# Performance work log

Hardware: AMD Instinct MI355X
Metric: run time of the kernel (lower is better)

## Reference

```python
import jax, jax.numpy as jnp
import numpy as np

N = 50000      # total nodes
E = 800000     # edges (before self loops)
B = 512        # graphs in batch
NODE_F = 9
GLOB_F = 4
IN_F = 13
H = 4          # heads
C = 16         # per-head channels (64 // 4)
HID = 64
NEG_SLOPE = 0.2


def setup_inputs() -> dict:
    key = jax.random.key(0)
    ks = jax.random.split(key, 32)
    inp = {}
    inp["node_feats"] = jax.random.normal(ks[0], (N, NODE_F), jnp.float32)
    inp["x_global_features"] = jax.random.normal(ks[1], (B, GLOB_F), jnp.float32)
    inp["edge_index"] = jax.random.randint(ks[2], (2, E), 0, N, jnp.int32)
    inp["batch_idx"] = jnp.sort(jax.random.randint(ks[3], (N,), 0, B, jnp.int32))
    dims = [IN_F, HID, HID]
    k = 4
    for l in range(3):
        s = 1.0 / np.sqrt(dims[l])
        inp[f"W{l}"] = jax.random.normal(ks[k], (dims[l], H * C), jnp.float32) * s; k += 1
        inp[f"att_src{l}"] = jax.random.normal(ks[k], (H, C), jnp.float32) * 0.1; k += 1
        inp[f"att_dst{l}"] = jax.random.normal(ks[k], (H, C), jnp.float32) * 0.1; k += 1
        inp[f"b{l}"] = jnp.zeros((H * C,), jnp.float32)
    mlp_dims = [(64, 64), (64, 64), (64, 64), (64, 1)]
    for i, (a, o) in enumerate(mlp_dims):
        inp[f"mlp_W{i}"] = jax.random.normal(ks[k], (a, o), jnp.float32) * (1.0 / np.sqrt(a)); k += 1
        inp[f"mlp_b{i}"] = jnp.zeros((o,), jnp.float32)
    return inp


def _gat_conv(x, src, dst, W, a_src, a_dst, bias, n):
    # h: [n, H, C]
    h = (x @ W).reshape(n, H, C)
    alpha_src = jnp.sum(h * a_src, axis=-1)   # [n, H]
    alpha_dst = jnp.sum(h * a_dst, axis=-1)   # [n, H]
    e = alpha_src[src] + alpha_dst[dst]       # [E', H]
    e = jax.nn.leaky_relu(e, NEG_SLOPE)
    # softmax over incoming edges per destination node (self loops guarantee >=1 edge)
    m = jax.ops.segment_max(e, dst, num_segments=n)
    e = jnp.exp(e - m[dst])
    s = jax.ops.segment_sum(e, dst, num_segments=n)
    alpha = e / s[dst]                        # [E', H]
    out = jax.ops.segment_sum(h[src] * alpha[:, :, None], dst, num_segments=n)
    return out.reshape(n, H * C) + bias


def _forward(node_feats, x_global_features,
             W0, att_src0, att_dst0, b0,
             W1, att_src1, att_dst1, b1,
             W2, att_src2, att_dst2, b2,
             mlp_W0, mlp_b0, mlp_W1, mlp_b1, mlp_W2, mlp_b2, mlp_W3, mlp_b3,
             edge_index, batch_idx):
    n = node_feats.shape[0]
    # concat per-graph global features onto each node
    x = jnp.concatenate([node_feats, x_global_features[batch_idx]], axis=1)  # [N, 13]
    loops = jnp.arange(n, dtype=edge_index.dtype)
    src = jnp.concatenate([edge_index[0], loops])
    dst = jnp.concatenate([edge_index[1], loops])
    x = jax.nn.relu(_gat_conv(x, src, dst, W0, att_src0, att_dst0, b0, n))
    x = jax.nn.relu(_gat_conv(x, src, dst, W1, att_src1, att_dst1, b1, n))
    x = _gat_conv(x, src, dst, W2, att_src2, att_dst2, b2, n)  # no act on last layer
    # scatter_mean over graphs
    sums = jax.ops.segment_sum(x, batch_idx, num_segments=B)
    cnt = jax.ops.segment_sum(jnp.ones((n,), x.dtype), batch_idx, num_segments=B)
    pooled = sums / jnp.clip(cnt, 1.0)[:, None]               # [B, 64]
    h = jax.nn.relu(pooled @ mlp_W0 + mlp_b0)
    h = jax.nn.relu(h @ mlp_W1 + mlp_b1)
    h = jax.nn.relu(h @ mlp_W2 + mlp_b2)
    out = h @ mlp_W3 + mlp_b3                                  # [B, 1]
    return out.reshape(-1)                                     # flatten -> [B]


def reference(node_feats, x_global_features,
              W0, att_src0, att_dst0, b0,
              W1, att_src1, att_dst1, b1,
              W2, att_src2, att_dst2, b2,
              mlp_W0, mlp_b0, mlp_W1, mlp_b1, mlp_W2, mlp_b2, mlp_W3, mlp_b3,
              edge_index, batch_idx):
    return _forward(node_feats, x_global_features,
                    W0, att_src0, att_dst0, b0,
                    W1, att_src1, att_dst1, b1,
                    W2, att_src2, att_dst2, b2,
                    mlp_W0, mlp_b0, mlp_W1, mlp_b1, mlp_W2, mlp_b2, mlp_W3, mlp_b3,
                    edge_index, batch_idx)
```

## Files before the change

kernel.cpp:

```cpp
#include <hip/hip_runtime.h>
#include <hip/hip_fp16.h>

#define GAT_H 4
#define GAT_HC 64
#define NEG_SLOPE 0.2f
#define DB 128
#define NBMAX 512
#define CHUNK 4096
#define EPT 16

__device__ __forceinline__ float lrelu(float x) { return x >= 0.f ? x : NEG_SLOPE * x; }

template <int K, bool CONCAT>
__global__ __launch_bounds__(256) void gemm_attn(
    const float* __restrict__ x, const float* __restrict__ nf,
    const float* __restrict__ gf, const int* __restrict__ batch,
    const float* __restrict__ W,
    const float* __restrict__ att_s, const float* __restrict__ att_d,
    __half* __restrict__ h, float* __restrict__ asrc, float* __restrict__ adst,
    int N, int nwaves)
{
    int lane = threadIdx.x & 63;
    int wid = blockIdx.x * 4 + __builtin_amdgcn_readfirstlane(threadIdx.x >> 6);

    float w[K];
    #pragma unroll
    for (int k = 0; k < K; ++k) w[k] = W[k * 64 + lane];
    float as_c = att_s[lane];
    float ad_c = att_d[lane];

    for (int row = wid; row < N; row += nwaves) {
        float acc = 0.f;
        if (CONCAT) {
            #pragma unroll
            for (int k = 0; k < 9; ++k) acc = fmaf(nf[row * 9 + k], w[k], acc);
            int b = batch[row];
            #pragma unroll
            for (int k = 0; k < 4; ++k) acc = fmaf(gf[b * 4 + k], w[9 + k], acc);
        } else {
            #pragma unroll
            for (int k = 0; k < K; ++k) acc = fmaf(x[(size_t)row * K + k], w[k], acc);
        }
        h[(unsigned)row * 64u + (unsigned)lane] = __float2half(acc);
        float vs = acc * as_c;
        float vd = acc * ad_c;
        #pragma unroll
        for (int off = 8; off; off >>= 1) { vs += __shfl_xor(vs, off); vd += __shfl_xor(vd, off); }
        if ((lane & 15) == 0) {
            asrc[row * GAT_H + (lane >> 4)] = vs;
            adst[row * GAT_H + (lane >> 4)] = vd;
        }
    }
}


__global__ __launch_bounds__(256) void zero_small(unsigned* __restrict__ bin_cnt,
                                                  unsigned* __restrict__ bin_fill)
{
    int t = threadIdx.x;
    bin_cnt[t] = 0; bin_cnt[t + 256] = 0;
    bin_fill[t] = 0; bin_fill[t + 256] = 0;
}

__global__ __launch_bounds__(256) void hist_bins(const int* __restrict__ dst,
                                                 unsigned* __restrict__ bin_cnt, int E)
{
    __shared__ unsigned lh[NBMAX];
    int t = threadIdx.x;
    lh[t] = 0; lh[t + 256] = 0;
    __syncthreads();
    for (int e = blockIdx.x * 256 + t; e < E; e += gridDim.x * 256)
        atomicAdd(&lh[((unsigned)dst[e]) >> 7], 1u);
    __syncthreads();
    unsigned v = lh[t];       if (v) atomicAdd(&bin_cnt[t], v);
    v = lh[t + 256];          if (v) atomicAdd(&bin_cnt[t + 256], v);
}

__global__ __launch_bounds__(256) void scan_bins(const unsigned* __restrict__ bin_cnt,
                                                 unsigned* __restrict__ bin_base,
                                                 int* __restrict__ indptr,
                                                 int nb, int N, int E)
{
    __shared__ unsigned buf[NBMAX];
    int t = threadIdx.x;
    buf[t] = (t < nb) ? bin_cnt[t] : 0u;
    buf[t + 256] = (t + 256 < nb) ? bin_cnt[t + 256] : 0u;
    __syncthreads();
    for (int off = 1; off < NBMAX; off <<= 1) {
        unsigned a = 0, b = 0;
        if (t >= off) a = buf[t - off];
        b = buf[t + 256 - off];
        __syncthreads();
        buf[t] += a; buf[t + 256] += b;
        __syncthreads();
    }
    if (t == 0) { bin_base[0] = 0; indptr[N] = E; }
    if (t < nb) bin_base[t + 1] = buf[t];
    if (t + 256 < nb) bin_base[t + 257] = buf[t + 256];
}

__global__ __launch_bounds__(256) void bin_scatter(const int* __restrict__ src,
                                                   const int* __restrict__ dst,
                                                   const unsigned* __restrict__ bin_base,
                                                   unsigned* __restrict__ bin_fill,
                                                   unsigned* __restrict__ binned, int E)
{
    __shared__ unsigned lh[NBMAX];
    __shared__ int goff[NBMAX];
    __shared__ unsigned sorted[CHUNK];
    int t = threadIdx.x;
    lh[t] = 0; lh[t + 256] = 0;
    __syncthreads();
    int e0 = blockIdx.x * CHUNK;

    unsigned pk[EPT]; int bn[EPT]; unsigned rk[EPT];
    #pragma unroll
    for (int i = 0; i < EPT; ++i) {
        int e = e0 + i * 256 + t;
        bn[i] = -1;
        if (e < E) {
            unsigned d = (unsigned)dst[e];
            pk[i] = (d << 16) | (unsigned)src[e];
            bn[i] = (int)(d >> 7);
            rk[i] = atomicAdd(&lh[bn[i]], 1u);
        }
    }
    __syncthreads();
    unsigned c0 = lh[t], c1 = lh[t + 256];
    for (int off = 1; off < NBMAX; off <<= 1) {
        unsigned a = 0, b = 0;
        if (t >= off) a = lh[t - off];
        b = lh[t + 256 - off];
        __syncthreads();
        lh[t] += a; lh[t + 256] += b;
        __syncthreads();
    }
    unsigned x0 = lh[t] - c0, x1 = lh[t + 256] - c1;
    if (c0) { unsigned g = atomicAdd(&bin_fill[t], c0);
              goff[t] = (int)(bin_base[t] + g) - (int)x0; }
    if (c1) { unsigned g = atomicAdd(&bin_fill[t + 256], c1);
              goff[t + 256] = (int)(bin_base[t + 256] + g) - (int)x1; }
    lh[t] = x0; lh[t + 256] = x1;
    __syncthreads();
    #pragma unroll
    for (int i = 0; i < EPT; ++i)
        if (bn[i] >= 0) sorted[lh[bn[i]] + rk[i]] = pk[i];
    __syncthreads();
    int T = min(CHUNK, E - e0);
    for (int j = t; j < T; j += 256) {
        unsigned p = sorted[j];
        binned[goff[p >> 23] + j] = p;
    }
}

__global__ __launch_bounds__(256) void bin_finalize(const unsigned* __restrict__ binned,
                                                    const unsigned* __restrict__ bin_base,
                                                    int* __restrict__ csr_src,
                                                    int* __restrict__ indptr, int N)
{
    __shared__ unsigned lh[DB];
    __shared__ unsigned fill[DB];
    int t = threadIdx.x, b = blockIdx.x;
    unsigned base = bin_base[b];
    unsigned cnt = bin_base[b + 1] - base;
    if (t < DB) lh[t] = 0;
    __syncthreads();
    for (unsigned i = t; i < cnt; i += 256)
        atomicAdd(&lh[(binned[base + i] >> 16) & (DB - 1)], 1u);
    __syncthreads();
    unsigned c0 = (t < DB) ? lh[t] : 0;
    for (int off = 1; off < DB; off <<= 1) {
        unsigned a = 0;
        if (t >= off && t < DB) a = lh[t - off];
        __syncthreads();
        if (t < DB) lh[t] += a;
        __syncthreads();
    }
    if (t < DB) {
        unsigned excl = lh[t] - c0;
        int d = b * DB + t;
        if (d < N) indptr[d] = (int)(base + excl);
        fill[t] = excl;
    }
    __syncthreads();
    for (unsigned i = t; i < cnt; i += 256) {
        unsigned p = binned[base + i];
        unsigned pos = atomicAdd(&fill[(p >> 16) & (DB - 1)], 1u);
        csr_src[base + pos] = (int)(p & 0xFFFFu);
    }
}

template <bool RELU>
__global__ __launch_bounds__(256) void aggregate(
    const __half* __restrict__ h, const float* __restrict__ asrc,
    const float* __restrict__ adst, const int* __restrict__ indptr,
    const int* __restrict__ csr_src, const float* __restrict__ bias,
    float* __restrict__ xout, int N, int nwaves)
{
    int lane = threadIdx.x & 63;
    int wid = blockIdx.x * 4 + __builtin_amdgcn_readfirstlane(threadIdx.x >> 6);
    unsigned h16 = (unsigned)(lane >> 4);
    float bias_c = bias[lane];

    for (int node = wid; node < N; node += nwaves) {
        int beg = __builtin_amdgcn_readfirstlane(indptr[node]);
        int end = __builtin_amdgcn_readfirstlane(indptr[node + 1]);
        unsigned un = (unsigned)node;

        float adst_n = adst[un * 4u + h16];
        float p0 = __expf(lrelu(asrc[un * 4u + h16] + adst_n));
        float sacc = p0;
        float acc = __half2float(h[un * 64u + (unsigned)lane]) * p0;

        int e = beg;
        for (; e + 16 <= end; e += 16) {
            int s[16]; float a[16], hv[16];
            #pragma unroll
            for (int i = 0; i < 16; ++i) s[i] = csr_src[e + i];
            #pragma unroll
            for (int i = 0; i < 16; ++i) a[i] = asrc[(unsigned)s[i] * 4u + h16];
            #pragma unroll
            for (int i = 0; i < 16; ++i)
                hv[i] = __half2float(h[(unsigned)s[i] * 64u + (unsigned)lane]);
            #pragma unroll
            for (int i = 0; i < 16; ++i) {
                float p = __expf(lrelu(a[i] + adst_n));
                sacc += p;
                acc = fmaf(hv[i], p, acc);
            }
        }
        for (; e + 8 <= end; e += 8) {
            int s[8]; float a[8], hv[8];
            #pragma unroll
            for (int i = 0; i < 8; ++i) s[i] = csr_src[e + i];
            #pragma unroll
            for (int i = 0; i < 8; ++i) a[i] = asrc[(unsigned)s[i] * 4u + h16];
            #pragma unroll
            for (int i = 0; i < 8; ++i)
                hv[i] = __half2float(h[(unsigned)s[i] * 64u + (unsigned)lane]);
            #pragma unroll
            for (int i = 0; i < 8; ++i) {
                float p = __expf(lrelu(a[i] + adst_n));
                sacc += p;
                acc = fmaf(hv[i], p, acc);
            }
        }
        for (; e + 2 <= end; e += 2) {
            int s0 = csr_src[e], s1 = csr_src[e + 1];
            float a0 = asrc[(unsigned)s0 * 4u + h16];
            float a1 = asrc[(unsigned)s1 * 4u + h16];
            float h0 = __half2float(h[(unsigned)s0 * 64u + (unsigned)lane]);
            float h1 = __half2float(h[(unsigned)s1 * 64u + (unsigned)lane]);
            float pa = __expf(lrelu(a0 + adst_n));
            float pb = __expf(lrelu(a1 + adst_n));
            sacc += pa + pb;
            acc = fmaf(h0, pa, acc);
            acc = fmaf(h1, pb, acc);
        }
        if (e < end) {
            int s = csr_src[e];
            float p = __expf(lrelu(asrc[(unsigned)s * 4u + h16] + adst_n));
            sacc += p;
            acc = fmaf(__half2float(h[(unsigned)s * 64u + (unsigned)lane]), p, acc);
        }

        float o = acc / sacc + bias_c;
        if (RELU) o = fmaxf(o, 0.f);
        xout[un * 64u + (unsigned)lane] = o;
    }
}

__global__ void pool_mlp(const float* __restrict__ x, const int* __restrict__ batch, int N,
                         const float* __restrict__ W0, const float* __restrict__ b0,
                         const float* __restrict__ W1, const float* __restrict__ b1,
                         const float* __restrict__ W2, const float* __restrict__ b2,
                         const float* __restrict__ W3, const float* __restrict__ b3,
                         float* __restrict__ out)
{
    __shared__ int bounds[2];
    __shared__ float red[4][64];
    __shared__ float hb[64];
    int b = blockIdx.x, t = threadIdx.x;

    if (t < 2) {
        int target = b + t;
        int lo = 0, hi = N;
        while (lo < hi) {
            int mid = (lo + hi) >> 1;
            if (batch[mid] < target) lo = mid + 1; else hi = mid;
        }
        bounds[t] = lo;
    }
    __syncthreads();
    int beg = bounds[0], end = bounds[1];

    int c = t & 63, w = t >> 6;
    float sum = 0.f;
    for (int n = beg + w; n < end; n += 4) sum += x[(size_t)n * 64 + c];
    red[w][c] = sum;
    __syncthreads();
    if (t < 64) {
        float v = red[0][t] + red[1][t] + red[2][t] + red[3][t];
        float cb = fmaxf((float)(end - beg), 1.0f);
        hb[t] = v / cb;
    }
    __syncthreads();

    float v0 = 0.f;
    if (t < 64) {
        v0 = b0[t];
        for (int k = 0; k < 64; ++k) v0 = fmaf(hb[k], W0[k * 64 + t], v0);
        v0 = fmaxf(v0, 0.f);
    }
    __syncthreads(); if (t < 64) hb[t] = v0; __syncthreads();
    if (t < 64) {
        v0 = b1[t];
        for (int k = 0; k < 64; ++k) v0 = fmaf(hb[k], W1[k * 64 + t], v0);
        v0 = fmaxf(v0, 0.f);
    }
    __syncthreads(); if (t < 64) hb[t] = v0; __syncthreads();
    if (t < 64) {
        v0 = b2[t];
        for (int k = 0; k < 64; ++k) v0 = fmaf(hb[k], W2[k * 64 + t], v0);
        v0 = fmaxf(v0, 0.f);
    }
    __syncthreads(); if (t < 64) hb[t] = v0; __syncthreads();
    if (t < 64) {
        float r = hb[t] * W3[t];
        #pragma unroll
        for (int off = 32; off; off >>= 1) r += __shfl_xor(r, off);
        if (t == 0) out[b] = r + b3[0];
    }
}

extern "C" void kernel_launch(void* const* d_in, const int* in_sizes, int n_in,
                              void* d_out, int out_size, void* d_ws, size_t ws_size,
                              hipStream_t stream)
{
    const float* node_feats = (const float*)d_in[0];
    const float* glob       = (const float*)d_in[1];
    const int*   edge_index = (const int*)d_in[2];
    const int*   batch      = (const int*)d_in[3];
    const float* W[3]  = {(const float*)d_in[4],  (const float*)d_in[8],  (const float*)d_in[12]};
    const float* As[3] = {(const float*)d_in[5],  (const float*)d_in[9],  (const float*)d_in[13]};
    const float* Ad[3] = {(const float*)d_in[6],  (const float*)d_in[10], (const float*)d_in[14]};
    const float* Bi[3] = {(const float*)d_in[7],  (const float*)d_in[11], (const float*)d_in[15]};
    const float* mW0 = (const float*)d_in[16]; const float* mb0 = (const float*)d_in[17];
    const float* mW1 = (const float*)d_in[18]; const float* mb1 = (const float*)d_in[19];
    const float* mW2 = (const float*)d_in[20]; const float* mb2 = (const float*)d_in[21];
    const float* mW3 = (const float*)d_in[22]; const float* mb3 = (const float*)d_in[23];
    float* out = (float*)d_out;

    int N = in_sizes[0] / 9;
    int E = in_sizes[2] / 2;
    int B = in_sizes[1] / 4;
    const int* esrc = edge_index;
    const int* edst = edge_index + E;
    int nb = (N + DB - 1) / DB;

    char* ws = (char*)d_ws;
    size_t off = 0;
    auto alloc = [&](size_t bytes) -> void* {
        void* p = ws + off;
        off = (off + bytes + 255) & ~(size_t)255;
        return p;
    };
    __half*   hbuf     = (__half*)alloc((size_t)N * 64 * 2);
    float*    xbuf     = (float*)alloc((size_t)N * 64 * 4);
    float*    asrc     = (float*)alloc((size_t)N * GAT_H * 4);
    float*    adst     = (float*)alloc((size_t)N * GAT_H * 4);
    int*      indptr   = (int*)alloc((size_t)(N + 1) * 4);
    int*      csr_src  = (int*)alloc((size_t)E * 4);
    unsigned* binned   = (unsigned*)alloc((size_t)E * 4);
    unsigned* bin_cnt  = (unsigned*)alloc(NBMAX * 4);
    unsigned* bin_base = (unsigned*)alloc((NBMAX + 1) * 4);
    unsigned* bin_fill = (unsigned*)alloc(NBMAX * 4);
    (void)ws_size;

    zero_small<<<1, 256, 0, stream>>>(bin_cnt, bin_fill);
    hist_bins<<<400, 256, 0, stream>>>(edst, bin_cnt, E);
    scan_bins<<<1, 256, 0, stream>>>(bin_cnt, bin_base, indptr, nb, N, E);
    bin_scatter<<<(E + CHUNK - 1) / CHUNK, 256, 0, stream>>>(esrc, edst, bin_base, bin_fill,
                                                             binned, E);
    bin_finalize<<<nb, 256, 0, stream>>>(binned, bin_base, csr_src, indptr, N);

    const int gemmBlocks = 1024;
    const int aggBlocks = 12500;
    gemm_attn<13, true><<<gemmBlocks, 256, 0, stream>>>(nullptr, node_feats, glob, batch,
                                                        W[0], As[0], Ad[0], hbuf, asrc, adst,
                                                        N, gemmBlocks * 4);
    aggregate<true><<<aggBlocks, 256, 0, stream>>>(hbuf, asrc, adst, indptr, csr_src, Bi[0],
                                                   xbuf, N, aggBlocks * 4);
    gemm_attn<64, false><<<gemmBlocks, 256, 0, stream>>>(xbuf, nullptr, nullptr, nullptr,
                                                         W[1], As[1], Ad[1], hbuf, asrc, adst,
                                                         N, gemmBlocks * 4);
    aggregate<true><<<aggBlocks, 256, 0, stream>>>(hbuf, asrc, adst, indptr, csr_src, Bi[1],
                                                   xbuf, N, aggBlocks * 4);
    gemm_attn<64, false><<<gemmBlocks, 256, 0, stream>>>(xbuf, nullptr, nullptr, nullptr,
                                                         W[2], As[2], Ad[2], hbuf, asrc, adst,
                                                         N, gemmBlocks * 4);
    aggregate<false><<<aggBlocks, 256, 0, stream>>>(hbuf, asrc, adst, indptr, csr_src, Bi[2],
                                                    xbuf, N, aggBlocks * 4);

    pool_mlp<<<B, 256, 0, stream>>>(xbuf, batch, N,
                                    mW0, mb0, mW1, mb1, mW2, mb2, mW3, mb3, out);
}
```

Measured before the change: 184.6 us.

## Process eight edges per wave in aggregation and drop global atomics in histogram

```diff
diff --git a/kernel.cpp b/kernel.cpp
--- a/kernel.cpp
+++ b/kernel.cpp
@@ -8,6 +8,7 @@
 #define NBMAX 512
 #define CHUNK 4096
 #define EPT 16
+#define SLICES 128
 
 __device__ __forceinline__ float lrelu(float x) { return x >= 0.f ? x : NEG_SLOPE * x; }
 
@@ -54,16 +55,8 @@
 }
 
 
-__global__ __launch_bounds__(256) void zero_small(unsigned* __restrict__ bin_cnt,
-                                                  unsigned* __restrict__ bin_fill)
-{
-    int t = threadIdx.x;
-    bin_cnt[t] = 0; bin_cnt[t + 256] = 0;
-    bin_fill[t] = 0; bin_fill[t + 256] = 0;
-}
-
 __global__ __launch_bounds__(256) void hist_bins(const int* __restrict__ dst,
-                                                 unsigned* __restrict__ bin_cnt, int E)
+                                                 unsigned* __restrict__ slices, int E)
 {
     __shared__ unsigned lh[NBMAX];
     int t = threadIdx.x;
@@ -72,19 +65,26 @@
     for (int e = blockIdx.x * 256 + t; e < E; e += gridDim.x * 256)
         atomicAdd(&lh[((unsigned)dst[e]) >> 7], 1u);
     __syncthreads();
-    unsigned v = lh[t];       if (v) atomicAdd(&bin_cnt[t], v);
-    v = lh[t + 256];          if (v) atomicAdd(&bin_cnt[t + 256], v);
-}
-
-__global__ __launch_bounds__(256) void scan_bins(const unsigned* __restrict__ bin_cnt,
+    unsigned* slice = slices + (size_t)blockIdx.x * NBMAX;
+    slice[t] = lh[t];
+    slice[t + 256] = lh[t + 256];
+}
+
+__global__ __launch_bounds__(256) void scan_bins(const unsigned* __restrict__ slices,
                                                  unsigned* __restrict__ bin_base,
+                                                 unsigned* __restrict__ bin_fill,
                                                  int* __restrict__ indptr,
-                                                 int nb, int N, int E)
+                                                 int nslices, int N, int E)
 {
     __shared__ unsigned buf[NBMAX];
     int t = threadIdx.x;
-    buf[t] = (t < nb) ? bin_cnt[t] : 0u;
-    buf[t + 256] = (t + 256 < nb) ? bin_cnt[t + 256] : 0u;
+    unsigned s0 = 0, s1 = 0;
+    for (int s = 0; s < nslices; ++s) {
+        s0 += slices[(size_t)s * NBMAX + t];
+        s1 += slices[(size_t)s * NBMAX + t + 256];
+    }
+    buf[t] = s0; buf[t + 256] = s1;
+    bin_fill[t] = 0; bin_fill[t + 256] = 0;
     __syncthreads();
     for (int off = 1; off < NBMAX; off <<= 1) {
         unsigned a = 0, b = 0;
@@ -95,8 +95,8 @@
         __syncthreads();
     }
     if (t == 0) { bin_base[0] = 0; indptr[N] = E; }
-    if (t < nb) bin_base[t + 1] = buf[t];
-    if (t + 256 < nb) bin_base[t + 257] = buf[t + 256];
+    bin_base[t + 1] = buf[t];
+    bin_base[t + 257] = buf[t + 256];
 }
 
 __global__ __launch_bounds__(256) void bin_scatter(const int* __restrict__ src,
@@ -187,6 +187,107 @@
         unsigned p = binned[base + i];
         unsigned pos = atomicAdd(&fill[(p >> 16) & (DB - 1)], 1u);
         csr_src[base + pos] = (int)(p & 0xFFFFu);
+    }
+}
+
+template <bool RELU>
+__global__ __launch_bounds__(256) void aggregate8(
+    const __half* __restrict__ h, const float* __restrict__ asrc,
+    const float* __restrict__ adst, const int* __restrict__ indptr,
+    const int* __restrict__ csr_src, const float* __restrict__ bias,
+    float* __restrict__ xout, int N, int nwaves)
+{
+    int lane = threadIdx.x & 63;
+    int eslot = lane >> 3;
+    unsigned c8 = (unsigned)(lane & 7);
+    unsigned head = c8 >> 1;
+    int wid = blockIdx.x * 4 + __builtin_amdgcn_readfirstlane(threadIdx.x >> 6);
+
+    float4 bias0 = *reinterpret_cast<const float4*>(bias + c8 * 8u);
+    float4 bias1 = *reinterpret_cast<const float4*>(bias + c8 * 8u + 4u);
+
+    for (int node = wid; node < N; node += nwaves) {
+        int beg = __builtin_amdgcn_readfirstlane(indptr[node]);
+        int end = __builtin_amdgcn_readfirstlane(indptr[node + 1]);
+        int total = (end - beg) + 1;
+
+        float adst_n = adst[(unsigned)node * 4u + head];
+        float sacc = 0.f;
+        float acc[8];
+        #pragma unroll
+        for (int j = 0; j < 8; ++j) acc[j] = 0.f;
+
+        int g = 0;
+        for (; g + 16 <= total; g += 16) {
+            int i0 = g + eslot;
+            int i1 = g + 8 + eslot;
+            int s0 = (i0 == 0) ? node : csr_src[beg + i0 - 1];
+            int s1 = csr_src[beg + i1 - 1];
+            float a0 = asrc[(unsigned)s0 * 4u + head];
+            float a1 = asrc[(unsigned)s1 * 4u + head];
+            uint4 hv0 = *reinterpret_cast<const uint4*>(h + (unsigned)s0 * 64u + c8 * 8u);
+            uint4 hv1 = *reinterpret_cast<const uint4*>(h + (unsigned)s1 * 64u + c8 * 8u);
+            float p0 = __expf(lrelu(a0 + adst_n));
+            float p1 = __expf(lrelu(a1 + adst_n));
+            sacc += p0 + p1;
+            const __half2* q0 = reinterpret_cast<const __half2*>(&hv0);
+            const __half2* q1 = reinterpret_cast<const __half2*>(&hv1);
+            #pragma unroll
+            for (int j = 0; j < 4; ++j) {
+                float2 f0 = __half22float2(q0[j]);
+                float2 f1 = __half22float2(q1[j]);
+                acc[2 * j]     = fmaf(f0.x, p0, acc[2 * j]);
+                acc[2 * j + 1] = fmaf(f0.y, p0, acc[2 * j + 1]);
+                acc[2 * j]     = fmaf(f1.x, p1, acc[2 * j]);
+                acc[2 * j + 1] = fmaf(f1.y, p1, acc[2 * j + 1]);
+            }
+        }
+        for (; g < total; g += 8) {
+            int idx = g + eslot;
+            if (idx < total) {
+                int s = (idx == 0) ? node : csr_src[beg + idx - 1];
+                float a = asrc[(unsigned)s * 4u + head];
+                uint4 hv = *reinterpret_cast<const uint4*>(h + (unsigned)s * 64u + c8 * 8u);
+                float p = __expf(lrelu(a + adst_n));
+                sacc += p;
+                const __half2* q = reinterpret_cast<const __half2*>(&hv);
+                #pragma unroll
+                for (int j = 0; j < 4; ++j) {
+                    float2 f = __half22float2(q[j]);
+                    acc[2 * j]     = fmaf(f.x, p, acc[2 * j]);
+                    acc[2 * j + 1] = fmaf(f.y, p, acc[2 * j + 1]);
+                }
+            }
+        }
+
+        #pragma unroll
+        for (int off = 8; off <= 32; off <<= 1) {
+            sacc += __shfl_xor(sacc, off);
+            #pragma unroll
+            for (int j = 0; j < 8; ++j) acc[j] += __shfl_xor(acc[j], off);
+        }
+
+        if (eslot == 0) {
+            float inv = 1.0f / sacc;
+            float4 o0, o1;
+            o0.x = fmaf(acc[0], inv, bias0.x);
+            o0.y = fmaf(acc[1], inv, bias0.y);
+            o0.z = fmaf(acc[2], inv, bias0.z);
+            o0.w = fmaf(acc[3], inv, bias0.w);
+            o1.x = fmaf(acc[4], inv, bias1.x);
+            o1.y = fmaf(acc[5], inv, bias1.y);
+            o1.z = fmaf(acc[6], inv, bias1.z);
+            o1.w = fmaf(acc[7], inv, bias1.w);
+            if (RELU) {
+                o0.x = fmaxf(o0.x, 0.f); o0.y = fmaxf(o0.y, 0.f);
+                o0.z = fmaxf(o0.z, 0.f); o0.w = fmaxf(o0.w, 0.f);
+                o1.x = fmaxf(o1.x, 0.f); o1.y = fmaxf(o1.y, 0.f);
+                o1.z = fmaxf(o1.z, 0.f); o1.w = fmaxf(o1.w, 0.f);
+            }
+            float* op = xout + (unsigned)node * 64u + c8 * 8u;
+            *reinterpret_cast<float4*>(op) = o0;
+            *reinterpret_cast<float4*>(op + 4) = o1;
+        }
     }
 }
 
@@ -372,14 +473,13 @@
     int*      indptr   = (int*)alloc((size_t)(N + 1) * 4);
     int*      csr_src  = (int*)alloc((size_t)E * 4);
     unsigned* binned   = (unsigned*)alloc((size_t)E * 4);
-    unsigned* bin_cnt  = (unsigned*)alloc(NBMAX * 4);
+    unsigned* slices   = (unsigned*)alloc((size_t)SLICES * NBMAX * 4);
     unsigned* bin_base = (unsigned*)alloc((NBMAX + 1) * 4);
     unsigned* bin_fill = (unsigned*)alloc(NBMAX * 4);
     (void)ws_size;
 
-    zero_small<<<1, 256, 0, stream>>>(bin_cnt, bin_fill);
-    hist_bins<<<400, 256, 0, stream>>>(edst, bin_cnt, E);
-    scan_bins<<<1, 256, 0, stream>>>(bin_cnt, bin_base, indptr, nb, N, E);
+    hist_bins<<<SLICES, 256, 0, stream>>>(edst, slices, E);
+    scan_bins<<<1, 256, 0, stream>>>(slices, bin_base, bin_fill, indptr, SLICES, N, E);
     bin_scatter<<<(E + CHUNK - 1) / CHUNK, 256, 0, stream>>>(esrc, edst, bin_base, bin_fill,
                                                              binned, E);
     bin_finalize<<<nb, 256, 0, stream>>>(binned, bin_base, csr_src, indptr, N);
@@ -389,13 +489,13 @@
     gemm_attn<13, true><<<gemmBlocks, 256, 0, stream>>>(nullptr, node_feats, glob, batch,
                                                         W[0], As[0], Ad[0], hbuf, asrc, adst,
                                                         N, gemmBlocks * 4);
-    aggregate<true><<<aggBlocks, 256, 0, stream>>>(hbuf, asrc, adst, indptr, csr_src, Bi[0],
-                                                   xbuf, N, aggBlocks * 4);
+    aggregate8<true><<<aggBlocks, 256, 0, stream>>>(hbuf, asrc, adst, indptr, csr_src, Bi[0],
+                                                    xbuf, N, aggBlocks * 4);
     gemm_attn<64, false><<<gemmBlocks, 256, 0, stream>>>(xbuf, nullptr, nullptr, nullptr,
                                                          W[1], As[1], Ad[1], hbuf, asrc, adst,
                                                          N, gemmBlocks * 4);
-    aggregate<true><<<aggBlocks, 256, 0, stream>>>(hbuf, asrc, adst, indptr, csr_src, Bi[1],
-                                                   xbuf, N, aggBlocks * 4);
+    aggregate8<true><<<aggBlocks, 256, 0, stream>>>(hbuf, asrc, adst, indptr, csr_src, Bi[1],
+                                                    xbuf, N, aggBlocks * 4);
     gemm_attn<64, false><<<gemmBlocks, 256, 0, stream>>>(xbuf, nullptr, nullptr, nullptr,
                                                          W[2], As[2], Ad[2], hbuf, asrc, adst,
                                                          N, gemmBlocks * 4);
```

New measurement: 195.8 us. +6.0%, slower.
